# Performance work log

Hardware: AMD Instinct MI355X
Metric: run time of the kernel (lower is better)

## Reference

```python
import jax, jax.numpy as jnp
import numpy as np

B, Q, K, H = 8, 512, 512, 1024
NH, HD = 16, 64
MAX_REL = 512  # max_relative_positions


def setup_inputs() -> dict:
    key = jax.random.key(0)
    ks = jax.random.split(key, 16)
    s = 1.0 / np.sqrt(H)
    inp = {
        "query": jax.random.normal(ks[0], (B, Q, H), jnp.float32),
        "key": jax.random.normal(ks[1], (B, K, H), jnp.float32),
        "value": jax.random.normal(ks[2], (B, K, H), jnp.float32),
        "key_padding_mask": jax.random.randint(ks[3], (B, K), 0, 2, jnp.int32),
        "Wq": jax.random.normal(ks[4], (H, H), jnp.float32) * s,
        "bq": jnp.zeros((H,), jnp.float32),
        "Wk": jax.random.normal(ks[5], (H, H), jnp.float32) * s,
        "bk": jnp.zeros((H,), jnp.float32),
        "Wv": jax.random.normal(ks[6], (H, H), jnp.float32) * s,
        "bv": jnp.zeros((H,), jnp.float32),
        "Wo": jax.random.normal(ks[7], (H, H), jnp.float32) * s,
        "bo": jnp.zeros((H,), jnp.float32),
        "rel_table": jax.random.normal(ks[8], (2 * MAX_REL - 1, NH), jnp.float32) * 0.02,
        "local_bias": jax.random.normal(ks[9], (512, 512), jnp.float32) * 0.1,
        "log_scale": jnp.zeros((1,), jnp.float32),
        "attention_bias": jnp.zeros((1,), jnp.float32),
    }
    return inp


def reference(query, key, value, key_padding_mask, Wq, bq, Wk, bk, Wv, bv, Wo, bo,
              rel_table, local_bias, log_scale, attention_bias):
    # projections -> [B, NH, len, HD]
    q = (query @ Wq + bq).reshape(B, Q, NH, HD).transpose(0, 2, 1, 3)
    k = (key @ Wk + bk).reshape(B, K, NH, HD).transpose(0, 2, 1, 3)
    v = (value @ Wv + bv).reshape(B, K, NH, HD).transpose(0, 2, 1, 3)

    scores = jnp.einsum('bhqd,bhkd->bhqk', q, k) / jnp.sqrt(jnp.float32(HD))

    # relative position bias
    rel = jnp.arange(Q)[:, None] - jnp.arange(K)[None, :]
    bucket = jnp.clip(rel, -(MAX_REL - 1), MAX_REL - 1) + (MAX_REL - 1)
    rel_bias = rel_table[bucket]            # [Q, K, NH]
    scores = scores + rel_bias.transpose(2, 0, 1)[None]  # [1, NH, Q, K]

    # local bias (Q,K <= 512)
    scores = scores + local_bias[:Q, :K][None, None] * 0.05

    scale = jnp.clip(jnp.exp(log_scale), 1.0, 4.0)
    scores = scores * scale + attention_bias

    pad = (key_padding_mask == 0)[:, None, None, :]  # [B,1,1,K]
    scores = jnp.where(pad, -jnp.inf, scores)
    # clamp AFTER masking: -inf -> -50 (padded keys get tiny but nonzero weight)
    scores = jnp.clip(scores, -50.0, 50.0)

    attn = jax.nn.softmax(scores, axis=-1)
    out = jnp.einsum('bhqk,bhkd->bhqd', attn, v)
    out = out.transpose(0, 2, 1, 3).reshape(B, Q, H)
    out = out @ Wo + bo
    return out, attn
```

## Files before the change

kernel.cpp:

```cpp
#include <hip/hip_runtime.h>

#define B_ 8
#define LQ 512
#define LK 512
#define HDIM 1024
#define NH_ 16
#define HD_ 64

typedef unsigned short u16;
typedef __attribute__((ext_vector_type(4))) float f32x4;
typedef __attribute__((ext_vector_type(4))) int i32x4;
typedef __attribute__((ext_vector_type(8))) __bf16 bf16x8;

static __device__ __forceinline__ u16 f2bf(float f) {
    union { float f; unsigned u; } v; v.f = f;
    unsigned u = v.u;
    return (u16)((u + 0x7fffu + ((u >> 16) & 1u)) >> 16);
}

static __device__ __forceinline__ float bf2f(u16 u) {
    union { unsigned u; float f; } v; v.u = ((unsigned)u) << 16;
    return v.f;
}

static __device__ __forceinline__ void gload_lds16(const u16* g, u16* l) {
    __builtin_amdgcn_global_load_lds((const __attribute__((address_space(1))) unsigned*)g,
                                     (__attribute__((address_space(3))) unsigned*)l, 16, 0, 0);
}

__global__ __launch_bounds__(256) void xcast_kernel(
    const float* __restrict__ x0, const float* __restrict__ x1, const float* __restrict__ x2,
    u16* __restrict__ o0, u16* __restrict__ o1, u16* __restrict__ o2)
{
    const float* X; u16* O;
    switch (blockIdx.z) { case 0: X = x0; O = o0; break; case 1: X = x1; O = o1; break;
                          default: X = x2; O = o2; }
    int i = blockIdx.x * 256 + threadIdx.x;
    f32x4 v = ((const f32x4*)X)[i];
    union { u16 u[4]; unsigned long long ull; } p;
    p.u[0] = f2bf(v[0]); p.u[1] = f2bf(v[1]); p.u[2] = f2bf(v[2]); p.u[3] = f2bf(v[3]);
    ((unsigned long long*)O)[i] = p.ull;
}

__global__ void wcast_kernel(const float* __restrict__ w0, const float* __restrict__ w1,
                             const float* __restrict__ w2, const float* __restrict__ w3,
                             u16* __restrict__ o0, u16* __restrict__ o1,
                             u16* __restrict__ o2, u16* __restrict__ o3) {
    const float* W; u16* O;
    switch (blockIdx.z) { case 0: W = w0; O = o0; break; case 1: W = w1; O = o1; break;
                          case 2: W = w2; O = o2; break; default: W = w3; O = o3; }
    __shared__ float t[32][33];
    int tx = threadIdx.x, ty = threadIdx.y;
    int n0 = blockIdx.x * 32, k0 = blockIdx.y * 32;
#pragma unroll
    for (int i = 0; i < 4; i++) {
        int k = ty * 4 + i;
        t[k][tx] = W[(k0 + k) * HDIM + n0 + tx];
    }
    __syncthreads();
#pragma unroll
    for (int i = 0; i < 4; i++) {
        int n = ty * 4 + i;
        O[(n0 + n) * HDIM + k0 + tx] = f2bf(t[tx][n]);
    }
}

__global__ __launch_bounds__(256) void biasprep_kernel(
    const float* __restrict__ rel_table, const float* __restrict__ local_bias,
    const float* __restrict__ log_scale, const float* __restrict__ att_bias,
    u16* __restrict__ Tb)
{
    int idx = blockIdx.x * 256 + threadIdx.x;
    int base = idx * 8;
    int h = base >> 18;
    int rem = base & 262143;
    int qi = rem >> 9, ki0 = rem & 511;
    float scale = fminf(fmaxf(__expf(log_scale[0]), 1.0f), 4.0f);
    float ab = att_bias[0];
    union { u16 u[8]; i32x4 v; } o;
#pragma unroll
    for (int t = 0; t < 8; t++) {
        int ki = ki0 + t;
        float r = rel_table[(qi - ki + 511) * NH_ + h];
        float lb = local_bias[qi * 512 + ki];
        o.u[t] = f2bf((r + lb * 0.05f) * scale + ab);
    }
    *(i32x4*)&Tb[base] = o.v;
}

__global__ __launch_bounds__(256) void proj2_kernel(
    const u16* __restrict__ x0, const u16* __restrict__ x1, const u16* __restrict__ x2,
    const u16* __restrict__ wt0, const u16* __restrict__ wt1, const u16* __restrict__ wt2,
    const float* __restrict__ bi0, const float* __restrict__ bi1, const float* __restrict__ bi2,
    u16* __restrict__ ot0, u16* __restrict__ ot1, u16* __restrict__ ot2)
{
    __shared__ u16 As[128 * 64];
    __shared__ u16 Bs[128 * 64];
    int bid = blockIdx.x;
    int swz = (bid & 7) * 96 + (bid >> 3);
    int z = swz >> 8, rem = swz & 255;
    int Mb = (rem >> 3) * 128, Nb = (rem & 7) * 128;
    const u16* X; const u16* WT; const float* bias; u16* out;
    switch (z) {
        case 0: X = x0; WT = wt0; bias = bi0; out = ot0; break;
        case 1: X = x1; WT = wt1; bias = bi1; out = ot1; break;
        default: X = x2; WT = wt2; bias = bi2; out = ot2; break;
    }
    int tid = threadIdx.x, lane = tid & 63, w = tid >> 6;
    int wm = (w & 1) * 64, wn = (w >> 1) * 64;
    int r16 = lane & 15, kg = lane >> 4;
    int rsw = (r16 & 7) * 8;
    int srow = lane >> 3;
    int scol = 8 * ((lane & 7) ^ (lane >> 3));
    const u16* gA = X + (size_t)Mb * HDIM;
    const u16* gB = WT + (size_t)Nb * HDIM;

    f32x4 acc[4][4] = {};
    for (int k0 = 0; k0 < HDIM; k0 += 64) {
#pragma unroll
        for (int i = 0; i < 4; i++) {
            int c = w * 4 + i;
            int row = c * 8 + srow;
            gload_lds16(&gA[(size_t)row * HDIM + k0 + scol], &As[c * 512]);
            gload_lds16(&gB[(size_t)row * HDIM + k0 + scol], &Bs[c * 512]);
        }
        __syncthreads();
#pragma unroll
        for (int kk = 0; kk < 2; kk++) {
            int colp = (kk * 32 + kg * 8) ^ rsw;
            bf16x8 a[4], b[4];
#pragma unroll
            for (int mt = 0; mt < 4; mt++) a[mt] = *(const bf16x8*)&As[(wm + mt * 16 + r16) * 64 + colp];
#pragma unroll
            for (int nt = 0; nt < 4; nt++) b[nt] = *(const bf16x8*)&Bs[(wn + nt * 16 + r16) * 64 + colp];
#pragma unroll
            for (int mt = 0; mt < 4; mt++)
#pragma unroll
                for (int nt = 0; nt < 4; nt++)
                    acc[mt][nt] = __builtin_amdgcn_mfma_f32_16x16x32_bf16(a[mt], b[nt], acc[mt][nt], 0, 0, 0);
        }
        __syncthreads();
    }
    int cr = (lane >> 4) * 4, cc = lane & 15;
#pragma unroll
    for (int nt = 0; nt < 4; nt++) {
        int n = Nb + wn + nt * 16 + cc;
        float bv = bias[n];
        int h = n >> 6, d = n & 63;
#pragma unroll
        for (int mt = 0; mt < 4; mt++) {
#pragma unroll
            for (int j = 0; j < 4; j++) {
                int m = Mb + wm + mt * 16 + cr + j;
                int b = m >> 9, l = m & 511;
                out[(((b * NH_ + h) * LQ) + l) * HD_ + d] = f2bf(acc[mt][nt][j] + bv);
            }
        }
    }
}

__global__ void vtrans_kernel(const u16* __restrict__ vb, u16* __restrict__ vT) {
    int bh = blockIdx.z;
    int k0 = blockIdx.x * 32, d0 = blockIdx.y * 32;
    __shared__ u16 t[32][33];
    int tx = threadIdx.x, ty = threadIdx.y;
    const u16* src = vb + (size_t)bh * (LK * HD_);
    u16* dst = vT + (size_t)bh * (LK * HD_);
#pragma unroll
    for (int i = 0; i < 4; i++) {
        int k = ty * 4 + i;
        t[k][tx] = src[(k0 + k) * HD_ + d0 + tx];
    }
    __syncthreads();
#pragma unroll
    for (int i = 0; i < 4; i++) {
        int d = ty * 4 + i;
        dst[(d0 + d) * LK + k0 + tx] = t[tx][d];
    }
}

__global__ __launch_bounds__(512) void attn2_kernel(
    const u16* __restrict__ qb, const u16* __restrict__ kb, const u16* __restrict__ vT,
    const int* __restrict__ kpm, const u16* __restrict__ Tb,
    const float* __restrict__ log_scale,
    float* __restrict__ attn_out, u16* __restrict__ ctx)
{
    __shared__ u16 Qs[32][72];
    __shared__ int pmask[512];
    __shared__ float red[2][32][8];
    __shared__ u16 P[32][520];
    __shared__ float pred[4][32][16];

    int bh = blockIdx.y;
    int q0 = blockIdx.x * 32;
    int b = bh >> 4, h = bh & 15;
    int tid = threadIdx.x, lane = tid & 63, w = tid >> 6;
    int r16 = lane & 15, kg = lane >> 4;

    float cscale = 0.125f * fminf(fmaxf(__expf(log_scale[0]), 1.0f), 4.0f);

    if (tid < 256) {
        int row = tid >> 3, c8 = tid & 7;
        *(i32x4*)&Qs[row][c8 * 8] = *(const i32x4*)&qb[((size_t)bh * LQ + q0 + row) * HD_ + c8 * 8];
    }
    pmask[tid & 511] = kpm[b * LK + (tid & 511)];
    __syncthreads();

    bf16x8 aq[2][2];
#pragma unroll
    for (int m = 0; m < 2; m++)
#pragma unroll
        for (int kk = 0; kk < 2; kk++)
            aq[m][kk] = *(const bf16x8*)&Qs[m * 16 + r16][kk * 32 + kg * 8];

    f32x4 acc[2][4] = {};
    const u16* kbase = kb + ((size_t)bh * LK + w * 64) * HD_;
#pragma unroll
    for (int nt = 0; nt < 4; nt++) {
        bf16x8 bk0 = *(const bf16x8*)&kbase[(nt * 16 + r16) * HD_ + kg * 8];
        bf16x8 bk1 = *(const bf16x8*)&kbase[(nt * 16 + r16) * HD_ + 32 + kg * 8];
#pragma unroll
        for (int m = 0; m < 2; m++) {
            acc[m][nt] = __builtin_amdgcn_mfma_f32_16x16x32_bf16(aq[m][0], bk0, acc[m][nt], 0, 0, 0);
            acc[m][nt] = __builtin_amdgcn_mfma_f32_16x16x32_bf16(aq[m][1], bk1, acc[m][nt], 0, 0, 0);
        }
    }

    const u16* Th = Tb + ((size_t)h << 18);
    float rm[2][4];
#pragma unroll
    for (int m = 0; m < 2; m++)
#pragma unroll
        for (int j = 0; j < 4; j++) rm[m][j] = -1e30f;
#pragma unroll
    for (int m = 0; m < 2; m++) {
#pragma unroll
        for (int nt = 0; nt < 4; nt++) {
            int ki = w * 64 + nt * 16 + r16;
            bool masked = (pmask[ki] == 0);
#pragma unroll
            for (int j = 0; j < 4; j++) {
                int row = m * 16 + kg * 4 + j;
                int qi = q0 + row;
                float s = fmaf(acc[m][nt][j], cscale, bf2f(Th[qi * 512 + ki]));
                s = fminf(fmaxf(s, -50.0f), 50.0f);
                s = masked ? -50.0f : s;
                acc[m][nt][j] = s;
                rm[m][j] = fmaxf(rm[m][j], s);
            }
        }
    }
#pragma unroll
    for (int m = 0; m < 2; m++)
#pragma unroll
        for (int j = 0; j < 4; j++) {
            float v = rm[m][j];
            v = fmaxf(v, __shfl_xor(v, 1));
            v = fmaxf(v, __shfl_xor(v, 2));
            v = fmaxf(v, __shfl_xor(v, 4));
            v = fmaxf(v, __shfl_xor(v, 8));
            rm[m][j] = v;
        }
    if (r16 == 0) {
#pragma unroll
        for (int m = 0; m < 2; m++)
#pragma unroll
            for (int j = 0; j < 4; j++) red[0][m * 16 + kg * 4 + j][w] = rm[m][j];
    }
    __syncthreads();
    float fm[2][4];
#pragma unroll
    for (int m = 0; m < 2; m++)
#pragma unroll
        for (int j = 0; j < 4; j++) {
            int row = m * 16 + kg * 4 + j;
            float v = red[0][row][0];
#pragma unroll
            for (int ww = 1; ww < 8; ww++) v = fmaxf(v, red[0][row][ww]);
            fm[m][j] = v;
        }
    float ps[2][4] = {};
#pragma unroll
    for (int m = 0; m < 2; m++)
#pragma unroll
        for (int nt = 0; nt < 4; nt++)
#pragma unroll
            for (int j = 0; j < 4; j++) {
                float e = __expf(acc[m][nt][j] - fm[m][j]);
                acc[m][nt][j] = e;
                ps[m][j] += e;
            }
#pragma unroll
    for (int m = 0; m < 2; m++)
#pragma unroll
        for (int j = 0; j < 4; j++) {
            float v = ps[m][j];
            v += __shfl_xor(v, 1);
            v += __shfl_xor(v, 2);
            v += __shfl_xor(v, 4);
            v += __shfl_xor(v, 8);
            ps[m][j] = v;
        }
    if (r16 == 0) {
#pragma unroll
        for (int m = 0; m < 2; m++)
#pragma unroll
            for (int j = 0; j < 4; j++) red[1][m * 16 + kg * 4 + j][w] = ps[m][j];
    }
    __syncthreads();

    float* dst = attn_out + ((size_t)bh * LQ + q0) * (size_t)LK + w * 64;
#pragma unroll
    for (int m = 0; m < 2; m++)
#pragma unroll
        for (int j = 0; j < 4; j++) {
            int row = m * 16 + kg * 4 + j;
            float sum = 0.f;
#pragma unroll
            for (int ww = 0; ww < 8; ww++) sum += red[1][row][ww];
            float inv = 1.0f / sum;
#pragma unroll
            for (int nt = 0; nt < 4; nt++) {
                float p = acc[m][nt][j] * inv;
                __builtin_nontemporal_store(p, &dst[(size_t)row * LK + nt * 16 + r16]);
                P[row][w * 64 + nt * 16 + r16] = f2bf(p);
            }
        }
    __syncthreads();

    int wd = (w & 3) * 16;
    int kh = (w >> 2) * 256;
    const u16* vbase = vT + (size_t)bh * (HD_ * LK);
    f32x4 po[2] = {};
#pragma unroll
    for (int kt = 0; kt < 8; kt++) {
        int k0 = kh + kt * 32;
        bf16x8 bvf = *(const bf16x8*)&vbase[(size_t)(wd + r16) * LK + k0 + kg * 8];
#pragma unroll
        for (int m = 0; m < 2; m++) {
            bf16x8 af = *(const bf16x8*)&P[m * 16 + r16][k0 + kg * 8];
            po[m] = __builtin_amdgcn_mfma_f32_16x16x32_bf16(af, bvf, po[m], 0, 0, 0);
        }
    }
    if (w >= 4) {
#pragma unroll
        for (int m = 0; m < 2; m++)
#pragma unroll
            for (int j = 0; j < 4; j++)
                pred[w & 3][m * 16 + kg * 4 + j][r16] = po[m][j];
    }
    __syncthreads();
    if (w < 4) {
#pragma unroll
        for (int m = 0; m < 2; m++)
#pragma unroll
            for (int j = 0; j < 4; j++) {
                int row = m * 16 + kg * 4 + j;
                float v = po[m][j] + pred[w][row][r16];
                ctx[((size_t)(b * LQ + q0 + row)) * HDIM + h * HD_ + wd + r16] = f2bf(v);
            }
    }
}

__global__ __launch_bounds__(256) void oproj2_kernel(
    const u16* __restrict__ ctx, const u16* __restrict__ WT,
    const float* __restrict__ bias, float* __restrict__ out)
{
    __shared__ u16 As[128 * 64];
    __shared__ u16 Bs[128 * 64];
    int bid = blockIdx.x;
    int idx = (bid & 7) * 32 + (bid >> 3);
    int Mb = (idx >> 3) * 128, Nb = (idx & 7) * 128;
    int tid = threadIdx.x, lane = tid & 63, w = tid >> 6;
    int wm = (w & 1) * 64, wn = (w >> 1) * 64;
    int r16 = lane & 15, kg = lane >> 4;
    int rsw = (r16 & 7) * 8;
    int srow = lane >> 3;
    int scol = 8 * ((lane & 7) ^ (lane >> 3));
    const u16* gA = ctx + (size_t)Mb * HDIM;
    const u16* gB = WT + (size_t)Nb * HDIM;

    f32x4 acc[4][4] = {};
    for (int k0 = 0; k0 < HDIM; k0 += 64) {
#pragma unroll
        for (int i = 0; i < 4; i++) {
            int c = w * 4 + i;
            int row = c * 8 + srow;
            gload_lds16(&gA[(size_t)row * HDIM + k0 + scol], &As[c * 512]);
            gload_lds16(&gB[(size_t)row * HDIM + k0 + scol], &Bs[c * 512]);
        }
        __syncthreads();
#pragma unroll
        for (int kk = 0; kk < 2; kk++) {
            int colp = (kk * 32 + kg * 8) ^ rsw;
            bf16x8 a[4], b[4];
#pragma unroll
            for (int mt = 0; mt < 4; mt++) a[mt] = *(const bf16x8*)&As[(wm + mt * 16 + r16) * 64 + colp];
#pragma unroll
            for (int nt = 0; nt < 4; nt++) b[nt] = *(const bf16x8*)&Bs[(wn + nt * 16 + r16) * 64 + colp];
#pragma unroll
            for (int mt = 0; mt < 4; mt++)
#pragma unroll
                for (int nt = 0; nt < 4; nt++)
                    acc[mt][nt] = __builtin_amdgcn_mfma_f32_16x16x32_bf16(a[mt], b[nt], acc[mt][nt], 0, 0, 0);
        }
        __syncthreads();
    }
    int cr = (lane >> 4) * 4, cc = lane & 15;
#pragma unroll
    for (int nt = 0; nt < 4; nt++) {
        int n = Nb + wn + nt * 16 + cc;
        float bv = bias[n];
#pragma unroll
        for (int mt = 0; mt < 4; mt++) {
#pragma unroll
            for (int j = 0; j < 4; j++) {
                int m = Mb + wm + mt * 16 + cr + j;
                out[(size_t)m * HDIM + n] = acc[mt][nt][j] + bv;
            }
        }
    }
}

extern "C" void kernel_launch(void* const* d_in, const int* in_sizes, int n_in,
                              void* d_out, int out_size, void* d_ws, size_t ws_size,
                              hipStream_t stream) {
    (void)in_sizes; (void)n_in; (void)out_size; (void)ws_size;
    const float* query = (const float*)d_in[0];
    const float* key_  = (const float*)d_in[1];
    const float* value = (const float*)d_in[2];
    const int*   kpm   = (const int*)d_in[3];
    const float* Wq = (const float*)d_in[4];  const float* bq = (const float*)d_in[5];
    const float* Wk = (const float*)d_in[6];  const float* bk = (const float*)d_in[7];
    const float* Wv = (const float*)d_in[8];  const float* bv = (const float*)d_in[9];
    const float* Wo = (const float*)d_in[10]; const float* bo = (const float*)d_in[11];
    const float* rel_table  = (const float*)d_in[12];
    const float* local_bias = (const float*)d_in[13];
    const float* log_scale  = (const float*)d_in[14];
    const float* att_bias   = (const float*)d_in[15];

    char* ws = (char*)d_ws;
    u16* WTq = (u16*)(ws + 0ull);
    u16* WTk = (u16*)(ws + (2ull << 20));
    u16* WTv = (u16*)(ws + (4ull << 20));
    u16* WTo = (u16*)(ws + (6ull << 20));
    u16* qb  = (u16*)(ws + (8ull << 20));
    u16* kb  = (u16*)(ws + (16ull << 20));
    u16* vb  = (u16*)(ws + (24ull << 20));
    u16* vT  = (u16*)(ws + (32ull << 20));
    u16* ctx = (u16*)(ws + (40ull << 20));
    u16* xq  = (u16*)(ws + (32ull << 20));
    u16* xk  = (u16*)(ws + (40ull << 20));
    u16* xv  = (u16*)(ws + (48ull << 20));
    u16* Tb  = (u16*)(ws + (48ull << 20));

    float* out  = (float*)d_out;
    float* attn = out + (size_t)4096 * 1024;

    xcast_kernel<<<dim3(4096, 1, 3), 256, 0, stream>>>(query, key_, value, xq, xk, xv);
    wcast_kernel<<<dim3(32, 32, 4), dim3(32, 8), 0, stream>>>(Wq, Wk, Wv, Wo, WTq, WTk, WTv, WTo);
    proj2_kernel<<<768, 256, 0, stream>>>(xq, xk, xv, WTq, WTk, WTv, bq, bk, bv, qb, kb, vb);
    vtrans_kernel<<<dim3(16, 2, 128), dim3(32, 8), 0, stream>>>(vb, vT);
    biasprep_kernel<<<2048, 256, 0, stream>>>(rel_table, local_bias, log_scale, att_bias, Tb);
    attn2_kernel<<<dim3(16, 128), 512, 0, stream>>>(qb, kb, vT, kpm, Tb, log_scale, attn, ctx);
    oproj2_kernel<<<256, 256, 0, stream>>>(ctx, WTo, bo, out);
}
```

Baseline: 167.8 us.

## Fuse V transpose into projection, use fixed softmax max, restructure PV

```diff
diff --git a/kernel.cpp b/kernel.cpp
--- a/kernel.cpp
+++ b/kernel.cpp
@@ -142,44 +142,42 @@
         __syncthreads();
     }
     int cr = (lane >> 4) * 4, cc = lane & 15;
-#pragma unroll
-    for (int nt = 0; nt < 4; nt++) {
-        int n = Nb + wn + nt * 16 + cc;
-        float bv = bias[n];
-        int h = n >> 6, d = n & 63;
-#pragma unroll
-        for (int mt = 0; mt < 4; mt++) {
-#pragma unroll
-            for (int j = 0; j < 4; j++) {
-                int m = Mb + wm + mt * 16 + cr + j;
-                int b = m >> 9, l = m & 511;
-                out[(((b * NH_ + h) * LQ) + l) * HD_ + d] = f2bf(acc[mt][nt][j] + bv);
+    if (z == 2) {
+#pragma unroll
+        for (int nt = 0; nt < 4; nt++) {
+            int n = Nb + wn + nt * 16 + cc;
+            float bv = bias[n];
+            int h = n >> 6, d = n & 63;
+#pragma unroll
+            for (int mt = 0; mt < 4; mt++) {
+#pragma unroll
+                for (int j = 0; j < 4; j++) {
+                    int m = Mb + wm + mt * 16 + cr + j;
+                    int b = m >> 9, l = m & 511;
+                    out[((size_t)(b * NH_ + h) * HD_ + d) * LK + l] = f2bf(acc[mt][nt][j] + bv);
+                }
             }
         }
-    }
-}
-
-__global__ void vtrans_kernel(const u16* __restrict__ vb, u16* __restrict__ vT) {
-    int bh = blockIdx.z;
-    int k0 = blockIdx.x * 32, d0 = blockIdx.y * 32;
-    __shared__ u16 t[32][33];
-    int tx = threadIdx.x, ty = threadIdx.y;
-    const u16* src = vb + (size_t)bh * (LK * HD_);
-    u16* dst = vT + (size_t)bh * (LK * HD_);
-#pragma unroll
-    for (int i = 0; i < 4; i++) {
-        int k = ty * 4 + i;
-        t[k][tx] = src[(k0 + k) * HD_ + d0 + tx];
-    }
-    __syncthreads();
-#pragma unroll
-    for (int i = 0; i < 4; i++) {
-        int d = ty * 4 + i;
-        dst[(d0 + d) * LK + k0 + tx] = t[tx][d];
-    }
-}
-
-__global__ __launch_bounds__(512) void attn2_kernel(
+    } else {
+#pragma unroll
+        for (int nt = 0; nt < 4; nt++) {
+            int n = Nb + wn + nt * 16 + cc;
+            float bv = bias[n];
+            int h = n >> 6, d = n & 63;
+#pragma unroll
+            for (int mt = 0; mt < 4; mt++) {
+#pragma unroll
+                for (int j = 0; j < 4; j++) {
+                    int m = Mb + wm + mt * 16 + cr + j;
+                    int b = m >> 9, l = m & 511;
+                    out[(((b * NH_ + h) * LQ) + l) * HD_ + d] = f2bf(acc[mt][nt][j] + bv);
+                }
+            }
+        }
+    }
+}
+
+__global__ __launch_bounds__(512) void attn3_kernel(
     const u16* __restrict__ qb, const u16* __restrict__ kb, const u16* __restrict__ vT,
     const int* __restrict__ kpm, const u16* __restrict__ Tb,
     const float* __restrict__ log_scale,
@@ -187,9 +185,8 @@
 {
     __shared__ u16 Qs[32][72];
     __shared__ int pmask[512];
-    __shared__ float red[2][32][8];
-    __shared__ u16 P[32][520];
-    __shared__ float pred[4][32][16];
+    __shared__ float red[32][8];
+    __shared__ u16 P[32][516];
 
     int bh = blockIdx.y;
     int q0 = blockIdx.x * 32;
@@ -227,11 +224,7 @@
     }
 
     const u16* Th = Tb + ((size_t)h << 18);
-    float rm[2][4];
-#pragma unroll
-    for (int m = 0; m < 2; m++)
-#pragma unroll
-        for (int j = 0; j < 4; j++) rm[m][j] = -1e30f;
+    float ps[2][4] = {};
 #pragma unroll
     for (int m = 0; m < 2; m++) {
 #pragma unroll
@@ -245,51 +238,13 @@
                 float s = fmaf(acc[m][nt][j], cscale, bf2f(Th[qi * 512 + ki]));
                 s = fminf(fmaxf(s, -50.0f), 50.0f);
                 s = masked ? -50.0f : s;
-                acc[m][nt][j] = s;
-                rm[m][j] = fmaxf(rm[m][j], s);
-            }
-        }
-    }
-#pragma unroll
-    for (int m = 0; m < 2; m++)
-#pragma unroll
-        for (int j = 0; j < 4; j++) {
-            float v = rm[m][j];
-            v = fmaxf(v, __shfl_xor(v, 1));
-            v = fmaxf(v, __shfl_xor(v, 2));
-            v = fmaxf(v, __shfl_xor(v, 4));
-            v = fmaxf(v, __shfl_xor(v, 8));
-            rm[m][j] = v;
-        }
-    if (r16 == 0) {
-#pragma unroll
-        for (int m = 0; m < 2; m++)
-#pragma unroll
-            for (int j = 0; j < 4; j++) red[0][m * 16 + kg * 4 + j][w] = rm[m][j];
-    }
-    __syncthreads();
-    float fm[2][4];
-#pragma unroll
-    for (int m = 0; m < 2; m++)
-#pragma unroll
-        for (int j = 0; j < 4; j++) {
-            int row = m * 16 + kg * 4 + j;
-            float v = red[0][row][0];
-#pragma unroll
-            for (int ww = 1; ww < 8; ww++) v = fmaxf(v, red[0][row][ww]);
-            fm[m][j] = v;
-        }
-    float ps[2][4] = {};
-#pragma unroll
-    for (int m = 0; m < 2; m++)
-#pragma unroll
-        for (int nt = 0; nt < 4; nt++)
-#pragma unroll
-            for (int j = 0; j < 4; j++) {
-                float e = __expf(acc[m][nt][j] - fm[m][j]);
+                float e = __expf(s - 50.0f);
                 acc[m][nt][j] = e;
                 ps[m][j] += e;
+                P[row][w * 64 + nt * 16 + r16] = f2bf(e);
             }
+        }
+    }
 #pragma unroll
     for (int m = 0; m < 2; m++)
 #pragma unroll
@@ -305,60 +260,47 @@
 #pragma unroll
         for (int m = 0; m < 2; m++)
 #pragma unroll
-            for (int j = 0; j < 4; j++) red[1][m * 16 + kg * 4 + j][w] = ps[m][j];
+            for (int j = 0; j < 4; j++) red[m * 16 + kg * 4 + j][w] = ps[m][j];
     }
     __syncthreads();
 
-    float* dst = attn_out + ((size_t)bh * LQ + q0) * (size_t)LK + w * 64;
+    float inv[2][4];
 #pragma unroll
     for (int m = 0; m < 2; m++)
 #pragma unroll
         for (int j = 0; j < 4; j++) {
             int row = m * 16 + kg * 4 + j;
-            float sum = 0.f;
-#pragma unroll
-            for (int ww = 0; ww < 8; ww++) sum += red[1][row][ww];
-            float inv = 1.0f / sum;
-#pragma unroll
-            for (int nt = 0; nt < 4; nt++) {
-                float p = acc[m][nt][j] * inv;
-                __builtin_nontemporal_store(p, &dst[(size_t)row * LK + nt * 16 + r16]);
-                P[row][w * 64 + nt * 16 + r16] = f2bf(p);
-            }
-        }
-    __syncthreads();
-
-    int wd = (w & 3) * 16;
-    int kh = (w >> 2) * 256;
-    const u16* vbase = vT + (size_t)bh * (HD_ * LK);
-    f32x4 po[2] = {};
-#pragma unroll
-    for (int kt = 0; kt < 8; kt++) {
-        int k0 = kh + kt * 32;
-        bf16x8 bvf = *(const bf16x8*)&vbase[(size_t)(wd + r16) * LK + k0 + kg * 8];
-#pragma unroll
-        for (int m = 0; m < 2; m++) {
-            bf16x8 af = *(const bf16x8*)&P[m * 16 + r16][k0 + kg * 8];
-            po[m] = __builtin_amdgcn_mfma_f32_16x16x32_bf16(af, bvf, po[m], 0, 0, 0);
-        }
-    }
-    if (w >= 4) {
-#pragma unroll
-        for (int m = 0; m < 2; m++)
-#pragma unroll
-            for (int j = 0; j < 4; j++)
-                pred[w & 3][m * 16 + kg * 4 + j][r16] = po[m][j];
-    }
-    __syncthreads();
-    if (w < 4) {
-#pragma unroll
-        for (int m = 0; m < 2; m++)
-#pragma unroll
-            for (int j = 0; j < 4; j++) {
-                int row = m * 16 + kg * 4 + j;
-                float v = po[m][j] + pred[w][row][r16];
-                ctx[((size_t)(b * LQ + q0 + row)) * HDIM + h * HD_ + wd + r16] = f2bf(v);
-            }
+            f32x4 s0 = *(const f32x4*)&red[row][0];
+            f32x4 s1 = *(const f32x4*)&red[row][4];
+            float sum = (s0[0] + s0[1]) + (s0[2] + s0[3]) + (s1[0] + s1[1]) + (s1[2] + s1[3]);
+            inv[m][j] = __builtin_amdgcn_rcpf(sum);
+        }
+
+    float* dst = attn_out + ((size_t)bh * LQ + q0) * (size_t)LK + w * 64;
+#pragma unroll
+    for (int m = 0; m < 2; m++)
+#pragma unroll
+        for (int j = 0; j < 4; j++) {
+            int row = m * 16 + kg * 4 + j;
+#pragma unroll
+            for (int nt = 0; nt < 4; nt++)
+                __builtin_nontemporal_store(acc[m][nt][j] * inv[m][j],
+                                            &dst[(size_t)row * LK + nt * 16 + r16]);
+        }
+
+    int qh = w & 1, dt = w >> 1;
+    const u16* vbase = vT + ((size_t)bh * HD_ + dt * 16 + r16) * LK;
+    f32x4 po = {};
+#pragma unroll
+    for (int kt = 0; kt < 16; kt++) {
+        bf16x8 af = *(const bf16x8*)&P[qh * 16 + r16][kt * 32 + kg * 8];
+        bf16x8 bvf = *(const bf16x8*)&vbase[kt * 32 + kg * 8];
+        po = __builtin_amdgcn_mfma_f32_16x16x32_bf16(af, bvf, po, 0, 0, 0);
+    }
+#pragma unroll
+    for (int j = 0; j < 4; j++) {
+        int q = q0 + qh * 16 + kg * 4 + j;
+        ctx[((size_t)(b * LQ + q)) * HDIM + h * HD_ + dt * 16 + r16] = f2bf(po[j] * inv[qh][j]);
     }
 }
 
@@ -446,10 +388,9 @@
     u16* WTo = (u16*)(ws + (6ull << 20));
     u16* qb  = (u16*)(ws + (8ull << 20));
     u16* kb  = (u16*)(ws + (16ull << 20));
-    u16* vb  = (u16*)(ws + (24ull << 20));
-    u16* vT  = (u16*)(ws + (32ull << 20));
+    u16* vT  = (u16*)(ws + (24ull << 20));
+    u16* xq  = (u16*)(ws + (32ull << 20));
     u16* ctx = (u16*)(ws + (40ull << 20));
-    u16* xq  = (u16*)(ws + (32ull << 20));
     u16* xk  = (u16*)(ws + (40ull << 20));
     u16* xv  = (u16*)(ws + (48ull << 20));
     u16* Tb  = (u16*)(ws + (48ull << 20));
@@ -459,9 +400,8 @@
 
     xcast_kernel<<<dim3(4096, 1, 3), 256, 0, stream>>>(query, key_, value, xq, xk, xv);
     wcast_kernel<<<dim3(32, 32, 4), dim3(32, 8), 0, stream>>>(Wq, Wk, Wv, Wo, WTq, WTk, WTv, WTo);
-    proj2_kernel<<<768, 256, 0, stream>>>(xq, xk, xv, WTq, WTk, WTv, bq, bk, bv, qb, kb, vb);
-    vtrans_kernel<<<dim3(16, 2, 128), dim3(32, 8), 0, stream>>>(vb, vT);
+    proj2_kernel<<<768, 256, 0, stream>>>(xq, xk, xv, WTq, WTk, WTv, bq, bk, bv, qb, kb, vT);
     biasprep_kernel<<<2048, 256, 0, stream>>>(rel_table, local_bias, log_scale, att_bias, Tb);
-    attn2_kernel<<<dim3(16, 128), 512, 0, stream>>>(qb, kb, vT, kpm, Tb, log_scale, attn, ctx);
+    attn3_kernel<<<dim3(16, 128), 512, 0, stream>>>(qb, kb, vT, kpm, Tb, log_scale, attn, ctx);
     oproj2_kernel<<<256, 256, 0, stream>>>(ctx, WTo, bo, out);
 }
```

Result: slower. 182.1 us (+8.6%).

## Transpose bias table, prefetch bias and V into registers, swizzle attention blocks

Applied to the files above, without the earlier changes.

```diff
diff --git a/kernel.cpp b/kernel.cpp
--- a/kernel.cpp
+++ b/kernel.cpp
@@ -8,6 +8,7 @@
 #define HD_ 64
 
 typedef unsigned short u16;
+typedef unsigned long long u64;
 typedef __attribute__((ext_vector_type(4))) float f32x4;
 typedef __attribute__((ext_vector_type(4))) int i32x4;
 typedef __attribute__((ext_vector_type(8))) __bf16 bf16x8;
@@ -37,9 +38,9 @@
                           default: X = x2; O = o2; }
     int i = blockIdx.x * 256 + threadIdx.x;
     f32x4 v = ((const f32x4*)X)[i];
-    union { u16 u[4]; unsigned long long ull; } p;
+    union { u16 u[4]; u64 ull; } p;
     p.u[0] = f2bf(v[0]); p.u[1] = f2bf(v[1]); p.u[2] = f2bf(v[2]); p.u[3] = f2bf(v[3]);
-    ((unsigned long long*)O)[i] = p.ull;
+    ((u64*)O)[i] = p.ull;
 }
 
 __global__ void wcast_kernel(const float* __restrict__ w0, const float* __restrict__ w1,
@@ -74,13 +75,13 @@
     int base = idx * 8;
     int h = base >> 18;
     int rem = base & 262143;
-    int qi = rem >> 9, ki0 = rem & 511;
+    int ki = rem >> 9, qi0 = rem & 511;
     float scale = fminf(fmaxf(__expf(log_scale[0]), 1.0f), 4.0f);
     float ab = att_bias[0];
     union { u16 u[8]; i32x4 v; } o;
 #pragma unroll
     for (int t = 0; t < 8; t++) {
-        int ki = ki0 + t;
+        int qi = qi0 + t;
         float r = rel_table[(qi - ki + 511) * NH_ + h];
         float lb = local_bias[qi * 512 + ki];
         o.u[t] = f2bf((r + lb * 0.05f) * scale + ab);
@@ -179,7 +180,7 @@
     }
 }
 
-__global__ __launch_bounds__(512) void attn2_kernel(
+__global__ __launch_bounds__(512, 4) void attn5_kernel(
     const u16* __restrict__ qb, const u16* __restrict__ kb, const u16* __restrict__ vT,
     const int* __restrict__ kpm, const u16* __restrict__ Tb,
     const float* __restrict__ log_scale,
@@ -191,14 +192,33 @@
     __shared__ u16 P[32][520];
     __shared__ float pred[4][32][16];
 
-    int bh = blockIdx.y;
-    int q0 = blockIdx.x * 32;
+    int bid = blockIdx.x;
+    int swz = (bid & 7) * 256 + (bid >> 3);
+    int bh = swz >> 4;
+    int q0 = (swz & 15) * 32;
     int b = bh >> 4, h = bh & 15;
     int tid = threadIdx.x, lane = tid & 63, w = tid >> 6;
     int r16 = lane & 15, kg = lane >> 4;
 
     float cscale = 0.125f * fminf(fmaxf(__expf(log_scale[0]), 1.0f), 4.0f);
 
+    const u16* Th = Tb + ((size_t)h << 18);
+    u64 tvv[2][4];
+#pragma unroll
+    for (int m = 0; m < 2; m++)
+#pragma unroll
+        for (int nt = 0; nt < 4; nt++) {
+            int ki = w * 64 + nt * 16 + r16;
+            tvv[m][nt] = *(const u64*)&Th[(size_t)ki * 512 + q0 + m * 16 + kg * 4];
+        }
+    int wd = (w & 3) * 16;
+    int kh = (w >> 2) * 256;
+    const u16* vbase = vT + ((size_t)bh * HD_ + wd + r16) * LK;
+    bf16x8 vreg[8];
+#pragma unroll
+    for (int kt = 0; kt < 8; kt++)
+        vreg[kt] = *(const bf16x8*)&vbase[kh + kt * 32 + kg * 8];
+
     if (tid < 256) {
         int row = tid >> 3, c8 = tid & 7;
         *(i32x4*)&Qs[row][c8 * 8] = *(const i32x4*)&qb[((size_t)bh * LQ + q0 + row) * HD_ + c8 * 8];
@@ -226,7 +246,6 @@
         }
     }
 
-    const u16* Th = Tb + ((size_t)h << 18);
     float rm[2][4];
 #pragma unroll
     for (int m = 0; m < 2; m++)
@@ -238,11 +257,10 @@
         for (int nt = 0; nt < 4; nt++) {
             int ki = w * 64 + nt * 16 + r16;
             bool masked = (pmask[ki] == 0);
+            union { u64 ull; u16 u[4]; } tv; tv.ull = tvv[m][nt];
 #pragma unroll
             for (int j = 0; j < 4; j++) {
-                int row = m * 16 + kg * 4 + j;
-                int qi = q0 + row;
-                float s = fmaf(acc[m][nt][j], cscale, bf2f(Th[qi * 512 + ki]));
+                float s = fmaf(acc[m][nt][j], cscale, bf2f(tv.u[j]));
                 s = fminf(fmaxf(s, -50.0f), 50.0f);
                 s = masked ? -50.0f : s;
                 acc[m][nt][j] = s;
@@ -328,20 +346,18 @@
         }
     __syncthreads();
 
-    int wd = (w & 3) * 16;
-    int kh = (w >> 2) * 256;
-    const u16* vbase = vT + (size_t)bh * (HD_ * LK);
     f32x4 po[2] = {};
+    __builtin_amdgcn_s_setprio(1);
 #pragma unroll
     for (int kt = 0; kt < 8; kt++) {
         int k0 = kh + kt * 32;
-        bf16x8 bvf = *(const bf16x8*)&vbase[(size_t)(wd + r16) * LK + k0 + kg * 8];
 #pragma unroll
         for (int m = 0; m < 2; m++) {
             bf16x8 af = *(const bf16x8*)&P[m * 16 + r16][k0 + kg * 8];
-            po[m] = __builtin_amdgcn_mfma_f32_16x16x32_bf16(af, bvf, po[m], 0, 0, 0);
-        }
-    }
+            po[m] = __builtin_amdgcn_mfma_f32_16x16x32_bf16(af, vreg[kt], po[m], 0, 0, 0);
+        }
+    }
+    __builtin_amdgcn_s_setprio(0);
     if (w >= 4) {
 #pragma unroll
         for (int m = 0; m < 2; m++)
@@ -447,10 +463,10 @@
     u16* qb  = (u16*)(ws + (8ull << 20));
     u16* kb  = (u16*)(ws + (16ull << 20));
     u16* vb  = (u16*)(ws + (24ull << 20));
+    u16* xq  = (u16*)(ws + (32ull << 20));
     u16* vT  = (u16*)(ws + (32ull << 20));
+    u16* xk  = (u16*)(ws + (40ull << 20));
     u16* ctx = (u16*)(ws + (40ull << 20));
-    u16* xq  = (u16*)(ws + (32ull << 20));
-    u16* xk  = (u16*)(ws + (40ull << 20));
     u16* xv  = (u16*)(ws + (48ull << 20));
     u16* Tb  = (u16*)(ws + (48ull << 20));
 
@@ -462,6 +478,6 @@
     proj2_kernel<<<768, 256, 0, stream>>>(xq, xk, xv, WTq, WTk, WTv, bq, bk, bv, qb, kb, vb);
     vtrans_kernel<<<dim3(16, 2, 128), dim3(32, 8), 0, stream>>>(vb, vT);
     biasprep_kernel<<<2048, 256, 0, stream>>>(rel_table, local_bias, log_scale, att_bias, Tb);
-    attn2_kernel<<<dim3(16, 128), 512, 0, stream>>>(qb, kb, vT, kpm, Tb, log_scale, attn, ctx);
+    attn5_kernel<<<2048, 512, 0, stream>>>(qb, kb, vT, kpm, Tb, log_scale, attn, ctx);
     oproj2_kernel<<<256, 256, 0, stream>>>(ctx, WTo, bo, out);
 }
```

After: 176.1 us. 5.0% more time.
